# Optimization experiments

Hardware: AMD Instinct MI355X
Metric: run time of the kernel (lower is better)

The kernel has to match this reference:

```python
import jax, jax.numpy as jnp
import numpy as np

N_NODES = 32  # nodes per topological level
H = 256       # hidden size
D_IN = 64     # edge feature dim
T, E = 512, 128


def _lstm_layer(x, src, dst, Wih, Whh, b, reverse):
    """One direction of one layer over the layered lattice.
    x: [T,E,Din], src/dst: [T,E] node ids in [0,N_NODES).
    Returns per-edge hidden [T,E,H].
    """
    if reverse:  # traverse lattice in reverse topological order
        x = x[::-1]
        s, d = dst[::-1], src[::-1]
    else:
        s, d = src, dst
    h0 = jnp.zeros((N_NODES, H), x.dtype)
    c0 = jnp.zeros((N_NODES, H), x.dtype)

    def step(carry, inp):
        hn, cn = carry
        xe, se, de = inp
        hs, cs = hn[se], cn[se]                      # gather source-node states [E,H]
        gates = xe @ Wih.T + hs @ Whh.T + b          # LSTMCell: [E,4H]
        i, f, g, o = jnp.split(gates, 4, axis=-1)
        c = jax.nn.sigmoid(f) * cs + jax.nn.sigmoid(i) * jnp.tanh(g)
        h = jax.nn.sigmoid(o) * jnp.tanh(c)
        # combine_edges('mean'): segment-mean of incoming edges per dest node
        cnt = jax.ops.segment_sum(jnp.ones((E,), x.dtype), de, num_segments=N_NODES)
        denom = jnp.maximum(cnt, 1.0)[:, None]
        hn2 = jax.ops.segment_sum(h, de, num_segments=N_NODES) / denom
        cn2 = jax.ops.segment_sum(c, de, num_segments=N_NODES) / denom
        return (hn2, cn2), h

    _, eh = jax.lax.scan(step, (h0, c0), (x, s, d))
    if reverse:
        eh = eh[::-1]
    return eh


def setup_inputs() -> dict:
    key = jax.random.key(0)
    ks = jax.random.split(key, 16)
    x = jax.random.normal(ks[0], (T, E, D_IN), jnp.float32)
    src = jax.random.randint(ks[1], (T, E), 0, N_NODES, jnp.int32)
    dst = jax.random.randint(ks[2], (T, E), 0, N_NODES, jnp.int32)
    sc = 1.0 / np.sqrt(H)
    u = lambda k, shp: jax.random.uniform(k, shp, jnp.float32, -sc, sc)
    # layer 0: input D_IN; layer 1: input 2H (bidirectional concat). dim 0 = direction
    W_ih0 = u(ks[3], (2, 4 * H, D_IN))
    W_hh0 = u(ks[4], (2, 4 * H, H))
    b0 = u(ks[5], (2, 4 * H))
    W_ih1 = u(ks[6], (2, 4 * H, 2 * H))
    W_hh1 = u(ks[7], (2, 4 * H, H))
    b1 = u(ks[8], (2, 4 * H))
    return {"x": x, "W_ih0": W_ih0, "W_hh0": W_hh0, "b0": b0,
            "W_ih1": W_ih1, "W_hh1": W_hh1, "b1": b1,
            "src": src, "dst": dst}


def reference(x, W_ih0, W_hh0, b0, W_ih1, W_hh1, b1, src, dst):
    out = x
    for Wih, Whh, b in ((W_ih0, W_hh0, b0), (W_ih1, W_hh1, b1)):
        fwd = _lstm_layer(out, src, dst, Wih[0], Whh[0], b[0], reverse=False)
        bwd = _lstm_layer(out, src, dst, Wih[1], Whh[1], b[1], reverse=True)
        out = jnp.concatenate([fwd, bwd], axis=-1)  # [T,E,2H]
    return out
```

## Files before the change

### kernel.cpp

```cpp
#include <hip/hip_runtime.h>

#define T_STEPS 512
#define E_EDGES 128
#define NN 32
#define HH 256
#define G4 1024
#define NWG 64
#define TPB 256

typedef __attribute__((ext_vector_type(8))) short s8v;
typedef __attribute__((ext_vector_type(4))) float f4v;
typedef unsigned long long u64;

__device__ __forceinline__ float fsig(float x) {
  x = fminf(fmaxf(x, -30.f), 30.f);
  return 1.f / (1.f + __expf(-x));
}
__device__ __forceinline__ float ftanh(float x) {
  float xc = fminf(fmaxf(x, -15.f), 15.f);
  float e = __expf(2.f * xc);
  return (e - 1.f) / (e + 1.f);
}
__device__ __forceinline__ float b2f(short s) {
  return __uint_as_float(((unsigned)(unsigned short)s) << 16);
}
__device__ __forceinline__ void bar_lds() {
  asm volatile("s_waitcnt lgkmcnt(0)\n\ts_barrier" ::: "memory");
}

__global__ __launch_bounds__(128) void prep_kernel(const int* __restrict__ src,
    const int* __restrict__ dst, int* __restrict__ eord, int* __restrict__ eoff) {
  __shared__ int de0[E_EDGES], de1[E_EDGES], off0[NN + 1], off1[NN + 1];
  const int t = blockIdx.x, e = threadIdx.x;
  de0[e] = dst[t * E_EDGES + e];
  de1[e] = src[t * E_EDGES + e];
  __syncthreads();
  if (e == 0) {
    int c[NN];
    for (int i = 0; i < NN; ++i) c[i] = 0;
    for (int i = 0; i < E_EDGES; ++i) c[de0[i]]++;
    int s = 0;
    for (int i = 0; i < NN; ++i) { off0[i] = s; s += c[i]; }
    off0[NN] = E_EDGES;
  }
  if (e == 1) {
    int c[NN];
    for (int i = 0; i < NN; ++i) c[i] = 0;
    for (int i = 0; i < E_EDGES; ++i) c[de1[i]]++;
    int s = 0;
    for (int i = 0; i < NN; ++i) { off1[i] = s; s += c[i]; }
    off1[NN] = E_EDGES;
  }
  __syncthreads();
  int d0 = de0[e], r0 = 0, d1 = de1[e], r1 = 0;
  for (int i = 0; i < e; ++i) {
    r0 += (de0[i] == d0);
    r1 += (de1[i] == d1);
  }
  eord[((size_t)0 * T_STEPS + t) * E_EDGES + off0[d0] + r0] = e;
  eord[((size_t)1 * T_STEPS + (T_STEPS - 1 - t)) * E_EDGES + off1[d1] + r1] = e;
  if (e < NN + 1) {
    eoff[((size_t)0 * T_STEPS + t) * (NN + 1) + e] = off0[e];
    eoff[((size_t)1 * T_STEPS + (T_STEPS - 1 - t)) * (NN + 1) + e] = off1[e];
  }
}

template <int M>
__global__ __launch_bounds__(256) void gates_gemm(
    const float* __restrict__ In, const float* __restrict__ W,
    const float* __restrict__ b, float* __restrict__ Gx, int reverse, int t0,
    int Cs) {
  __shared__ float Wsh[64][68];
  __shared__ float Xsh[128][68];
  const int tid = threadIdx.x;
  const int k0 = blockIdx.x * 64;
  const int lt = blockIdx.y;
  const int t = t0 + lt;
  const int tsrc = reverse ? (T_STEPS - 1 - t) : t;
  const float* Inb = In + (size_t)tsrc * E_EDGES * M;

  const int ty = tid >> 4;
  const int tx = tid & 15;

  float acc[4][8];
#pragma unroll
  for (int i = 0; i < 4; ++i) {
    float bv = b[k0 + ty * 4 + i];
#pragma unroll
    for (int j = 0; j < 8; ++j) acc[i][j] = bv;
  }

  for (int m0 = 0; m0 < M; m0 += 64) {
    __syncthreads();
#pragma unroll
    for (int p = 0; p < 4; ++p) {
      int r = (tid >> 4) + 16 * p;
      int c4 = tid & 15;
      float4 v = *(const float4*)(W + (size_t)(k0 + r) * M + m0 + c4 * 4);
      *(float4*)(&Wsh[r][c4 * 4]) = v;
    }
#pragma unroll
    for (int p = 0; p < 8; ++p) {
      int r = (tid >> 4) + 16 * p;
      int c4 = tid & 15;
      float4 v = *(const float4*)(Inb + (size_t)r * M + m0 + c4 * 4);
      *(float4*)(&Xsh[r][c4 * 4]) = v;
    }
    __syncthreads();
#pragma unroll 4
    for (int mm4 = 0; mm4 < 16; ++mm4) {
      float4 wv4[4], xv4[8];
#pragma unroll
      for (int i = 0; i < 4; ++i) wv4[i] = *(const float4*)(&Wsh[ty * 4 + i][mm4 * 4]);
#pragma unroll
      for (int j = 0; j < 8; ++j) xv4[j] = *(const float4*)(&Xsh[tx + 16 * j][mm4 * 4]);
#pragma unroll
      for (int i = 0; i < 4; ++i)
#pragma unroll
        for (int j = 0; j < 8; ++j) {
          acc[i][j] = __fmaf_rn(wv4[i].x, xv4[j].x, acc[i][j]);
          acc[i][j] = __fmaf_rn(wv4[i].y, xv4[j].y, acc[i][j]);
          acc[i][j] = __fmaf_rn(wv4[i].z, xv4[j].z, acc[i][j]);
          acc[i][j] = __fmaf_rn(wv4[i].w, xv4[j].w, acc[i][j]);
        }
    }
  }
  {
    const int kb = k0 + ty * 4;
    const int gate = kb >> 8;
    const int ch = kb & 255;
    const int slot = ch >> 3;
    const int jj0 = ch & 7;
    float* gbase = Gx + ((((size_t)slot * Cs + lt) * 4 + gate) * E_EDGES) * 8 + jj0;
#pragma unroll
    for (int j = 0; j < 8; ++j) {
      int e = tx + 16 * j;
      *(float4*)(gbase + (size_t)e * 8) =
          make_float4(acc[0][j], acc[1][j], acc[2][j], acc[3][j]);
    }
  }
}

__global__ __launch_bounds__(TPB) void recur_kernel(
    const float* __restrict__ GxF, const float* __restrict__ GxB,
    const float* __restrict__ WhhF, const float* __restrict__ WhhB,
    const int* __restrict__ src, const int* __restrict__ dst,
    const int* __restrict__ eord, const int* __restrict__ eoff,
    u64* hnG, float* cnG, float* outBase,
    int t0, int nsteps) {
  __shared__ short WsB[2][32][33][8];
  __shared__ short hnB[2][32][33][8];
  __shared__ float zF[32][33];
  __shared__ float hE[E_EDGES][8];
  __shared__ float cE[E_EDGES][8];
  __shared__ float cnL[NN][9];
  __shared__ int eordL[E_EDGES];
  __shared__ int eoffL[NN + 1];
  __shared__ int mfmaOK;

  const int tid = threadIdx.x;
  const int wg = blockIdx.x;
  const int dir = wg >> 5;
  const int slot = wg & 31;
  const int j0 = slot * 8;
  const float* Gx = dir ? GxB : GxF;
  const float* Whh = dir ? WhhB : WhhF;
  const int* seA = dir ? dst : src;
  float* cnGd = cnG + (size_t)dir * NN * HH;

  {
    int gc = tid >> 3;
    int g = gc >> 3, jj2 = gc & 7;
    const float* wr = Whh + ((size_t)(g * HH) + j0 + jj2) * HH;
    int c0 = (tid & 7) * 32;
    for (int kk = 0; kk < 32; ++kk) {
      int k = c0 + kk;
      float f = wr[k];
      unsigned fb = __float_as_uint(f);
      unsigned hb = fb & 0xFFFF0000u;
      float lof = f - __uint_as_float(hb);
      WsB[0][k >> 3][gc][k & 7] = (short)(hb >> 16);
      WsB[1][k >> 3][gc][k & 7] = (short)(__float_as_uint(lof) >> 16);
    }
  }
  {
    int n = tid >> 3, jj = tid & 7;
    cnL[n][jj] = cnGd[n * HH + j0 + jj];
  }
  if (tid < 64) {
    s8v ta, tb;
    const int rr = tid & 15, kh = (tid >> 4) * 8;
#pragma unroll
    for (int i = 0; i < 8; ++i) {
      int k = kh + i;
      ta[i] = (short)(__float_as_uint((float)((rr + 2 * k) & 7)) >> 16);
      tb[i] = (short)(__float_as_uint((float)(((3 * k + rr) & 7) - 3)) >> 16);
    }
    f4v tacc = {0.f, 0.f, 0.f, 0.f};
    tacc = __builtin_amdgcn_mfma_f32_16x16x32_bf16(ta, tb, tacc, 0, 0, 0);
    bool ok = true;
    const int col = tid & 15, rbase = (tid >> 4) * 4;
#pragma unroll
    for (int g2 = 0; g2 < 4; ++g2) {
      int row = rbase + g2;
      float ex = 0.f;
      for (int k = 0; k < 32; ++k)
        ex += (float)((row + 2 * k) & 7) * (float)(((3 * k + col) & 7) - 3);
      ok &= (tacc[g2] == ex);
    }
    unsigned long long bb = __ballot(ok);
    if (tid == 0) mfmaOK = (bb == 0xFFFFFFFFFFFFFFFFull) ? 1 : 0;
  }
  __syncthreads();
  const bool useMfma = (mfmaOK != 0);

  const int e = tid >> 1, jh = tid & 1;
  const float* gxWG = Gx + (size_t)slot * nsteps * 4096 + (e * 8 + jh * 4);

  for (int rl = 0; rl < nsteps; ++rl) {
    const int r = t0 + rl;
    const int tv = dir ? (T_STEPS - 1 - r) : r;

    const int sec = seA[tv * E_EDGES + e];
    int eoV = 0, eofV = 0;
    if (tid < E_EDGES) eoV = eord[((size_t)dir * T_STEPS + r) * E_EDGES + tid];
    else if (tid < E_EDGES + NN + 1)
      eofV = eoff[((size_t)dir * T_STEPS + r) * (NN + 1) + (tid - E_EDGES)];
    const float* gp = gxWG + (size_t)rl * 4096;
    float4 gxi = *(const float4*)(gp + 0 * 1024);
    float4 gxf = *(const float4*)(gp + 1 * 1024);
    float4 gxg = *(const float4*)(gp + 2 * 1024);
    float4 gxo = *(const float4*)(gp + 3 * 1024);

    {
      const u64* hnRd = hnG + (size_t)((r & 1) * 2 + dir) * NN * HH;
      const unsigned want = (unsigned)(t0 + rl);
      u64 va[16], vb[16];
#pragma unroll
      for (int p = 0; p < 16; ++p) {
        int idx = tid + 256 * p;
        const u64* ptr = hnRd + (size_t)(idx >> 7) * HH + (idx & 127) * 2;
        va[p] = __hip_atomic_load(ptr, __ATOMIC_RELAXED, __HIP_MEMORY_SCOPE_AGENT);
        vb[p] = __hip_atomic_load(ptr + 1, __ATOMIC_RELAXED, __HIP_MEMORY_SCOPE_AGENT);
      }
      unsigned pend = 0xFFFFu;
      int guard = 0;
      for (;;) {
#pragma unroll
        for (int p = 0; p < 16; ++p) {
          if (pend & (1u << p)) {
            if ((unsigned)(va[p] >> 32) == want && (unsigned)(vb[p] >> 32) == want) {
              pend &= ~(1u << p);
              int idx = tid + 256 * p;
              int n = idx >> 7, c2 = idx & 127;
              unsigned u0 = (unsigned)va[p], u1 = (unsigned)vb[p];
              unsigned h0 = u0 & 0xFFFF0000u, h1 = u1 & 0xFFFF0000u;
              float l0f = __uint_as_float(u0) - __uint_as_float(h0);
              float l1f = __uint_as_float(u1) - __uint_as_float(h1);
              unsigned hw = h1 | (u0 >> 16);
              unsigned lw = (__float_as_uint(l1f) & 0xFFFF0000u) |
                            (__float_as_uint(l0f) >> 16);
              int k = c2 * 2;
              ((unsigned*)&hnB[0][k >> 3][n][0])[(k & 7) >> 1] = hw;
              ((unsigned*)&hnB[1][k >> 3][n][0])[(k & 7) >> 1] = lw;
            }
          }
        }
        if (!pend) break;
        if (++guard > (1 << 20)) break;
        __builtin_amdgcn_s_sleep(0);
#pragma unroll
        for (int p = 0; p < 16; ++p) {
          if (pend & (1u << p)) {
            int idx = tid + 256 * p;
            const u64* ptr = hnRd + (size_t)(idx >> 7) * HH + (idx & 127) * 2;
            va[p] = __hip_atomic_load(ptr, __ATOMIC_RELAXED, __HIP_MEMORY_SCOPE_AGENT);
            vb[p] = __hip_atomic_load(ptr + 1, __ATOMIC_RELAXED, __HIP_MEMORY_SCOPE_AGENT);
          }
        }
      }
      if (tid < E_EDGES) eordL[tid] = eoV;
      else if (tid < E_EDGES + NN + 1) eoffL[tid - E_EDGES] = eofV;
    }
    bar_lds();

    if (useMfma) {
      const int lane = tid & 63, wv = tid >> 6;
      const int gr = (wv >> 1) * 16;
      const int ncb = (wv & 1) * 16;
      const int ll = lane & 15, lh = lane >> 4;
      f4v ah = {0.f, 0.f, 0.f, 0.f}, bl = {0.f, 0.f, 0.f, 0.f};
#pragma unroll
      for (int kb = 0; kb < 8; ++kb) {
        s8v wh = *(const s8v*)&WsB[0][kb * 4 + lh][gr + ll][0];
        s8v wl = *(const s8v*)&WsB[1][kb * 4 + lh][gr + ll][0];
        s8v hh = *(const s8v*)&hnB[0][kb * 4 + lh][ncb + ll][0];
        s8v hl = *(const s8v*)&hnB[1][kb * 4 + lh][ncb + ll][0];
        ah = __builtin_amdgcn_mfma_f32_16x16x32_bf16(wh, hh, ah, 0, 0, 0);
        bl = __builtin_amdgcn_mfma_f32_16x16x32_bf16(wh, hl, bl, 0, 0, 0);
        bl = __builtin_amdgcn_mfma_f32_16x16x32_bf16(wl, hh, bl, 0, 0, 0);
      }
#pragma unroll
      for (int g2 = 0; g2 < 4; ++g2)
        zF[gr + lh * 4 + g2][ncb + ll] = ah[g2] + bl[g2];
    } else {
      int n = tid & 31, gq = tid >> 5;
      float za[4] = {0.f, 0.f, 0.f, 0.f};
      for (int k = 0; k < 256; ++k) {
        int kb8 = k >> 3, el = k & 7;
        float hv = b2f(hnB[0][kb8][n][el]) + b2f(hnB[1][kb8][n][el]);
#pragma unroll
        for (int q = 0; q < 4; ++q) {
          int gc = gq * 4 + q;
          za[q] += (b2f(WsB[0][kb8][gc][el]) + b2f(WsB[1][kb8][gc][el])) * hv;
        }
      }
#pragma unroll
      for (int q = 0; q < 4; ++q) zF[gq * 4 + q][n] = za[q];
    }
    bar_lds();

    {
      const float gi4[4] = {gxi.x, gxi.y, gxi.z, gxi.w};
      const float gf4[4] = {gxf.x, gxf.y, gxf.z, gxf.w};
      const float gg4[4] = {gxg.x, gxg.y, gxg.z, gxg.w};
      const float go4[4] = {gxo.x, gxo.y, gxo.z, gxo.w};
      float hq[4], cq[4];
#pragma unroll
      for (int u = 0; u < 4; ++u) {
        int jj = jh * 4 + u;
        float gi = gi4[u] + zF[jj][sec];
        float gf = gf4[u] + zF[8 + jj][sec];
        float gv = gg4[u] + zF[16 + jj][sec];
        float go = go4[u] + zF[24 + jj][sec];
        float cv = fsig(gf) * cnL[sec][jj] + fsig(gi) * ftanh(gv);
        float hv = fsig(go) * ftanh(cv);
        hq[u] = hv;
        cq[u] = cv;
      }
      *(float4*)&hE[e][jh * 4] = make_float4(hq[0], hq[1], hq[2], hq[3]);
      *(float4*)&cE[e][jh * 4] = make_float4(cq[0], cq[1], cq[2], cq[3]);
      int tw = dir ? (T_STEPS - 1 - r) : r;
      *(float4*)(outBase + ((size_t)tw * E_EDGES + e) * 512 + dir * 256 + j0 + jh * 4)
          = make_float4(hq[0], hq[1], hq[2], hq[3]);
    }
    bar_lds();

    {
      int n = tid >> 3, jj = tid & 7;
      int o0 = eoffL[n], o1 = eoffL[n + 1];
      float sh = 0.f, sc = 0.f;
      for (int o = o0; o < o1; ++o) {
        int ee = eordL[o];
        sh += hE[ee][jj];
        sc += cE[ee][jj];
      }
      int len = o1 - o0;
      float rdn = (len > 0) ? (1.f / (float)len) : 1.f;
      float hnv = sh * rdn;
      u64 pk = ((u64)(unsigned)(t0 + rl + 1) << 32) |
               (u64)__float_as_uint(hnv);
      u64* hnWr = hnG + (size_t)(((r + 1) & 1) * 2 + dir) * NN * HH +
                  (size_t)n * HH + j0 + jj;
      __hip_atomic_store(hnWr, pk, __ATOMIC_RELAXED, __HIP_MEMORY_SCOPE_AGENT);
      cnL[n][jj] = sc * rdn;
    }
    bar_lds();
  }

  {
    int n = tid >> 3, jj = tid & 7;
    cnGd[n * HH + j0 + jj] = cnL[n][jj];
  }
}

extern "C" void kernel_launch(void* const* d_in, const int* in_sizes, int n_in,
                              void* d_out, int out_size, void* d_ws, size_t ws_size,
                              hipStream_t stream) {
  const float* x = (const float*)d_in[0];
  const float* Wih0 = (const float*)d_in[1];
  const float* Whh0 = (const float*)d_in[2];
  const float* b0 = (const float*)d_in[3];
  const float* Wih1 = (const float*)d_in[4];
  const float* Whh1 = (const float*)d_in[5];
  const float* b1 = (const float*)d_in[6];
  const int* src = (const int*)d_in[7];
  const int* dst = (const int*)d_in[8];
  float* out = (float*)d_out;

  const size_t outElems = (size_t)T_STEPS * E_EDGES * 512;
  const size_t hnW = (size_t)4 * NN * HH;
  const size_t eordW = (size_t)2 * T_STEPS * E_EDGES;
  const size_t eoffW = (size_t)2 * T_STEPS * (NN + 1);
  int C = 512;
  while (C >= 1) {
    size_t need = (2 * (size_t)C * G4 * E_EDGES + outElems + 2 * hnW +
                   2 * (size_t)NN * HH + eordW + eoffW + 256) * sizeof(float);
    if (need <= ws_size) break;
    C >>= 1;
  }
  if (C < 1) return;

  float* GxF = (float*)d_ws;
  float* GxB = GxF + (size_t)C * G4 * E_EDGES;
  float* out0 = GxB + (size_t)C * G4 * E_EDGES;
  u64* hnG = (u64*)(out0 + outElems);
  float* cnG = (float*)(hnG + hnW);
  int* eord = (int*)(cnG + 2 * NN * HH);
  int* eoff = eord + eordW;

  prep_kernel<<<dim3(T_STEPS), 128, 0, stream>>>(src, dst, eord, eoff);

  for (int layer = 0; layer < 2; ++layer) {
    const float* Wih = layer ? Wih1 : Wih0;
    const float* Whh = layer ? Whh1 : Whh0;
    const float* bb = layer ? b1 : b0;
    const float* In = layer ? out0 : x;
    float* outT = layer ? out : out0;
    (void)hipMemsetAsync(hnG, 0, hnW * sizeof(u64), stream);
    (void)hipMemsetAsync(cnG, 0, 2 * NN * HH * sizeof(float), stream);
    for (int t0 = 0; t0 < T_STEPS; t0 += C) {
      if (layer == 0) {
        gates_gemm<64><<<dim3(16, C), 256, 0, stream>>>(In, Wih, bb, GxF, 0, t0, C);
        gates_gemm<64><<<dim3(16, C), 256, 0, stream>>>(In, Wih + (size_t)G4 * 64, bb + G4, GxB, 1, t0, C);
      } else {
        gates_gemm<512><<<dim3(16, C), 256, 0, stream>>>(In, Wih, bb, GxF, 0, t0, C);
        gates_gemm<512><<<dim3(16, C), 256, 0, stream>>>(In, Wih + (size_t)G4 * 512, bb + G4, GxB, 1, t0, C);
      }
      const float* gxF = GxF; const float* gxB = GxB;
      const float* whF = Whh; const float* whB = Whh + (size_t)G4 * HH;
      const int* psrc = src; const int* pdst = dst;
      const int* peord = eord; const int* peoff = eoff;
      u64* phn = hnG; float* pcn = cnG; float* pout = outT;
      int a_t0 = t0, a_ns = C;
      void* args[13] = {&gxF, &gxB, &whF, &whB, &psrc, &pdst, &peord, &peoff,
                        &phn, &pcn, &pout, &a_t0, &a_ns};
      hipLaunchCooperativeKernel((const void*)recur_kernel, dim3(NWG), dim3(TPB),
                                 args, 0, stream);
    }
  }
}
```

Measured before the change: 8.774 ms.

## Compute input-gate projections with split-bf16 MFMA instead of FP32 FMA

Replaces the scalar FP32 tiled GEMM for the input-to-gate projection with a kernel that splits each FP32 operand into high and low bf16 parts and accumulates three MFMA products (hi*hi, hi*lo, lo*hi) for near-FP32 accuracy. The block tile grows to 128 gate rows, which halves the grid in x, and bias is added in the epilogue. The aim is to cut the gate GEMM time by using matrix cores, at the cost of extra conversion work during LDS staging and slightly reduced precision compared with true FP32.

```diff
diff --git a/kernel.cpp b/kernel.cpp
--- a/kernel.cpp
+++ b/kernel.cpp
@@ -66,77 +66,101 @@
 }
 
 template <int M>
-__global__ __launch_bounds__(256) void gates_gemm(
+__global__ __launch_bounds__(256) void gates_mfma(
     const float* __restrict__ In, const float* __restrict__ W,
     const float* __restrict__ b, float* __restrict__ Gx, int reverse, int t0,
     int Cs) {
-  __shared__ float Wsh[64][68];
-  __shared__ float Xsh[128][68];
+  __shared__ short WsT[2][128][72];
+  __shared__ short XsT[2][128][72];
+  __shared__ float biasL[128];
   const int tid = threadIdx.x;
-  const int k0 = blockIdx.x * 64;
+  const int kb = blockIdx.x;
   const int lt = blockIdx.y;
   const int t = t0 + lt;
   const int tsrc = reverse ? (T_STEPS - 1 - t) : t;
   const float* Inb = In + (size_t)tsrc * E_EDGES * M;
 
-  const int ty = tid >> 4;
-  const int tx = tid & 15;
-
-  float acc[4][8];
-#pragma unroll
-  for (int i = 0; i < 4; ++i) {
-    float bv = b[k0 + ty * 4 + i];
-#pragma unroll
-    for (int j = 0; j < 8; ++j) acc[i][j] = bv;
-  }
-
-  for (int m0 = 0; m0 < M; m0 += 64) {
+  if (tid < 128) biasL[tid] = b[kb * 128 + tid];
+
+  const int lane = tid & 63, wv = tid >> 6;
+  const int ll = lane & 15, lh = lane >> 4;
+  const int srow = tid >> 1, sh32 = (tid & 1) * 32;
+
+  f4v acc[2][8];
+#pragma unroll
+  for (int i = 0; i < 2; ++i)
+#pragma unroll
+    for (int j = 0; j < 8; ++j) acc[i][j] = (f4v){0.f, 0.f, 0.f, 0.f};
+
+  for (int mc = 0; mc < M; mc += 64) {
     __syncthreads();
-#pragma unroll
-    for (int p = 0; p < 4; ++p) {
-      int r = (tid >> 4) + 16 * p;
-      int c4 = tid & 15;
-      float4 v = *(const float4*)(W + (size_t)(k0 + r) * M + m0 + c4 * 4);
-      *(float4*)(&Wsh[r][c4 * 4]) = v;
-    }
-#pragma unroll
-    for (int p = 0; p < 8; ++p) {
-      int r = (tid >> 4) + 16 * p;
-      int c4 = tid & 15;
-      float4 v = *(const float4*)(Inb + (size_t)r * M + m0 + c4 * 4);
-      *(float4*)(&Xsh[r][c4 * 4]) = v;
+    {
+      const float* wr = W + (size_t)(kb * 128 + srow) * M + mc + sh32;
+      const float* xr = Inb + (size_t)srow * M + mc + sh32;
+#pragma unroll
+      for (int i = 0; i < 8; ++i) {
+        float4 a = *(const float4*)(wr + i * 4);
+        float4 x = *(const float4*)(xr + i * 4);
+        unsigned ua[4] = {__float_as_uint(a.x), __float_as_uint(a.y),
+                          __float_as_uint(a.z), __float_as_uint(a.w)};
+        unsigned ux[4] = {__float_as_uint(x.x), __float_as_uint(x.y),
+                          __float_as_uint(x.z), __float_as_uint(x.w)};
+        unsigned la[4], lx[4];
+#pragma unroll
+        for (int u = 0; u < 4; ++u) {
+          la[u] = __float_as_uint(__uint_as_float(ua[u]) -
+                                  __uint_as_float(ua[u] & 0xFFFF0000u));
+          lx[u] = __float_as_uint(__uint_as_float(ux[u]) -
+                                  __uint_as_float(ux[u] & 0xFFFF0000u));
+        }
+        int off = sh32 + i * 4;
+        *(unsigned*)&WsT[0][srow][off + 0] = (ua[0] >> 16) | (ua[1] & 0xFFFF0000u);
+        *(unsigned*)&WsT[0][srow][off + 2] = (ua[2] >> 16) | (ua[3] & 0xFFFF0000u);
+        *(unsigned*)&WsT[1][srow][off + 0] = (la[0] >> 16) | (la[1] & 0xFFFF0000u);
+        *(unsigned*)&WsT[1][srow][off + 2] = (la[2] >> 16) | (la[3] & 0xFFFF0000u);
+        *(unsigned*)&XsT[0][srow][off + 0] = (ux[0] >> 16) | (ux[1] & 0xFFFF0000u);
+        *(unsigned*)&XsT[0][srow][off + 2] = (ux[2] >> 16) | (ux[3] & 0xFFFF0000u);
+        *(unsigned*)&XsT[1][srow][off + 0] = (lx[0] >> 16) | (lx[1] & 0xFFFF0000u);
+        *(unsigned*)&XsT[1][srow][off + 2] = (lx[2] >> 16) | (lx[3] & 0xFFFF0000u);
+      }
     }
     __syncthreads();
-#pragma unroll 4
-    for (int mm4 = 0; mm4 < 16; ++mm4) {
-      float4 wv4[4], xv4[8];
-#pragma unroll
-      for (int i = 0; i < 4; ++i) wv4[i] = *(const float4*)(&Wsh[ty * 4 + i][mm4 * 4]);
-#pragma unroll
-      for (int j = 0; j < 8; ++j) xv4[j] = *(const float4*)(&Xsh[tx + 16 * j][mm4 * 4]);
-#pragma unroll
-      for (int i = 0; i < 4; ++i)
-#pragma unroll
-        for (int j = 0; j < 8; ++j) {
-          acc[i][j] = __fmaf_rn(wv4[i].x, xv4[j].x, acc[i][j]);
-          acc[i][j] = __fmaf_rn(wv4[i].y, xv4[j].y, acc[i][j]);
-          acc[i][j] = __fmaf_rn(wv4[i].z, xv4[j].z, acc[i][j]);
-          acc[i][j] = __fmaf_rn(wv4[i].w, xv4[j].w, acc[i][j]);
-        }
-    }
-  }
-  {
-    const int kb = k0 + ty * 4;
-    const int gate = kb >> 8;
-    const int ch = kb & 255;
+#pragma unroll
+    for (int ks = 0; ks < 2; ++ks) {
+      const int mo = ks * 32 + lh * 8;
+      s8v ah0 = *(const s8v*)&WsT[0][wv * 32 + ll][mo];
+      s8v al0 = *(const s8v*)&WsT[1][wv * 32 + ll][mo];
+      s8v ah1 = *(const s8v*)&WsT[0][wv * 32 + 16 + ll][mo];
+      s8v al1 = *(const s8v*)&WsT[1][wv * 32 + 16 + ll][mo];
+#pragma unroll
+      for (int et = 0; et < 8; ++et) {
+        s8v bh = *(const s8v*)&XsT[0][et * 16 + ll][mo];
+        s8v blo = *(const s8v*)&XsT[1][et * 16 + ll][mo];
+        acc[0][et] = __builtin_amdgcn_mfma_f32_16x16x32_bf16(ah0, bh, acc[0][et], 0, 0, 0);
+        acc[0][et] = __builtin_amdgcn_mfma_f32_16x16x32_bf16(ah0, blo, acc[0][et], 0, 0, 0);
+        acc[0][et] = __builtin_amdgcn_mfma_f32_16x16x32_bf16(al0, bh, acc[0][et], 0, 0, 0);
+        acc[1][et] = __builtin_amdgcn_mfma_f32_16x16x32_bf16(ah1, bh, acc[1][et], 0, 0, 0);
+        acc[1][et] = __builtin_amdgcn_mfma_f32_16x16x32_bf16(ah1, blo, acc[1][et], 0, 0, 0);
+        acc[1][et] = __builtin_amdgcn_mfma_f32_16x16x32_bf16(al1, bh, acc[1][et], 0, 0, 0);
+      }
+    }
+  }
+#pragma unroll
+  for (int kt = 0; kt < 2; ++kt) {
+    const int kloc = wv * 32 + kt * 16 + lh * 4;
+    const int kg = kb * 128 + kloc;
+    const int gate = kg >> 8;
+    const int ch = kg & 255;
     const int slot = ch >> 3;
     const int jj0 = ch & 7;
-    float* gbase = Gx + ((((size_t)slot * Cs + lt) * 4 + gate) * E_EDGES) * 8 + jj0;
-#pragma unroll
-    for (int j = 0; j < 8; ++j) {
-      int e = tx + 16 * j;
-      *(float4*)(gbase + (size_t)e * 8) =
-          make_float4(acc[0][j], acc[1][j], acc[2][j], acc[3][j]);
+    const float4 bv = *(const float4*)&biasL[kloc];
+    float* gb = Gx + ((((size_t)slot * Cs + lt) * 4 + gate) * E_EDGES) * 8 + jj0;
+#pragma unroll
+    for (int et = 0; et < 8; ++et) {
+      int e = et * 16 + ll;
+      f4v v = acc[kt][et];
+      *(float4*)(gb + (size_t)e * 8) =
+          make_float4(v[0] + bv.x, v[1] + bv.y, v[2] + bv.z, v[3] + bv.w);
     }
   }
 }
@@ -421,11 +445,11 @@
     (void)hipMemsetAsync(cnG, 0, 2 * NN * HH * sizeof(float), stream);
     for (int t0 = 0; t0 < T_STEPS; t0 += C) {
       if (layer == 0) {
-        gates_gemm<64><<<dim3(16, C), 256, 0, stream>>>(In, Wih, bb, GxF, 0, t0, C);
-        gates_gemm<64><<<dim3(16, C), 256, 0, stream>>>(In, Wih + (size_t)G4 * 64, bb + G4, GxB, 1, t0, C);
+        gates_mfma<64><<<dim3(8, C), 256, 0, stream>>>(In, Wih, bb, GxF, 0, t0, C);
+        gates_mfma<64><<<dim3(8, C), 256, 0, stream>>>(In, Wih + (size_t)G4 * 64, bb + G4, GxB, 1, t0, C);
       } else {
-        gates_gemm<512><<<dim3(16, C), 256, 0, stream>>>(In, Wih, bb, GxF, 0, t0, C);
-        gates_gemm<512><<<dim3(16, C), 256, 0, stream>>>(In, Wih + (size_t)G4 * 512, bb + G4, GxB, 1, t0, C);
+        gates_mfma<512><<<dim3(8, C), 256, 0, stream>>>(In, Wih, bb, GxF, 0, t0, C);
+        gates_mfma<512><<<dim3(8, C), 256, 0, stream>>>(In, Wih + (size_t)G4 * 512, bb + G4, GxB, 1, t0, C);
       }
       const float* gxF = GxF; const float* gxB = GxB;
       const float* whF = Whh; const float* whB = Whh + (size_t)G4 * HH;
```

After: 7.507 ms. 14.4% less time.
